# Kernel optimization log

Hardware: AMD Instinct MI355X
Metric: run time of the kernel (lower is better)

Reference implementation:

```python
import jax, jax.numpy as jnp
import numpy as np

# levels for the auction iterations: j = 7..-1 gives level = -4^j, j = -2 gives level = 0
_LEVEL_JS = list(range(7, -3, -1))


def approx_match(xyz1, xyz2):
    # xyz1: [B,N,3], xyz2: [B,M,3] -> soft match matrix [B,N,M]
    B, N, _ = xyz1.shape
    M = xyz2.shape[1]
    multiL = 1.0 if N >= M else float(M // N)
    multiR = float(N // M) if N >= M else 1.0
    # pairwise squared distances [B,N,M]
    d2 = jnp.sum((xyz1[:, :, None, :] - xyz2[:, None, :, :]) ** 2, axis=-1)
    levels = jnp.array([0.0 if j == -2 else -(4.0 ** j) for j in _LEVEL_JS],
                       dtype=xyz1.dtype)

    def step(carry, level):
        match, remainL, remainR = carry
        w = jnp.exp(level * d2) * remainR[:, None, :]                      # [B,N,M]
        # row-normalize to each left point's remaining mass
        w = w * (remainL / (jnp.sum(w, axis=2) + 1e-9))[:, :, None]
        # clip columns to right points' remaining capacity
        ss = jnp.sum(w, axis=1) + 1e-9                                     # [B,M]
        w = w * jnp.minimum(remainR / ss, 1.0)[:, None, :]
        match = match + w
        remainL = jnp.maximum(remainL - jnp.sum(w, axis=2), 0.0)
        remainR = jnp.maximum(remainR - jnp.sum(w, axis=1), 0.0)
        return (match, remainL, remainR), None

    init = (jnp.zeros_like(d2),
            jnp.full((B, N), multiL, dtype=d2.dtype),
            jnp.full((B, M), multiR, dtype=d2.dtype))
    (match, _, _), _ = jax.lax.scan(step, init, levels)
    return match


def match_cost(xyz1, xyz2, match):
    # cost[b] = sum_{k,l} match[b,k,l] * ||xyz1[b,k] - xyz2[b,l]||
    d = jnp.sqrt(jnp.sum((xyz1[:, :, None, :] - xyz2[:, None, :, :]) ** 2, axis=-1))
    return jnp.sum(match * d, axis=(1, 2))


def setup_inputs() -> dict:
    key = jax.random.key(0)
    k1, k2 = jax.random.split(key)
    B, N, M = 8, 2048, 2048
    input1 = jax.random.normal(k1, (B, N, 3), dtype=jnp.float32)
    input2 = jax.random.normal(k2, (B, M, 3), dtype=jnp.float32)
    return {"input1": input1, "input2": input2}


def reference(input1, input2):
    match = approx_match(input1, input2)
    return match_cost(input1, input2, match)
```

## Files before the change

kernel.cpp:

```cpp
#include <hip/hip_runtime.h>
#include <hip/hip_fp16.h>


#define BATCH 8
#define NPTS 2048
#define MPTS 2048
#define BLOCK 1024
#define ROWS 64
#define BLOCKS_PER_BATCH 32
#define NSUB 8
#define SUBTGT (BLOCKS_PER_BATCH / NSUB)
#define NSYNC 21
#define PAD 16
#define SROW 17
#define LOG2E 1.44269504088896340736f

__device__ __forceinline__ float fast_exp2(float x) {
  return __builtin_amdgcn_exp2f(x);
}
__device__ __forceinline__ float fast_sqrt(float a) {
  return __builtin_amdgcn_sqrtf(a);
}
__device__ __forceinline__ float packh2(float c, float r) {
  __half2 h = __halves2half2(__float2half_rn(c), __float2half_rn(r));
  return __builtin_bit_cast(float, h);
}

__device__ __forceinline__ float cohLoad(const float* p) {
  return __hip_atomic_load((float*)p, __ATOMIC_RELAXED,
                           __HIP_MEMORY_SCOPE_AGENT);
}
__device__ __forceinline__ void cohStore(float* p, float v) {
  __hip_atomic_store(p, v, __ATOMIC_RELAXED, __HIP_MEMORY_SCOPE_AGENT);
}
__device__ __forceinline__ float4 cohLoad4(const float4* p) {
  const float* f = (const float*)p;
  return make_float4(cohLoad(f), cohLoad(f + 1), cohLoad(f + 2),
                     cohLoad(f + 3));
}

__device__ __forceinline__ void lds_barrier() {
  asm volatile("s_waitcnt lgkmcnt(0)" ::: "memory");
  __builtin_amdgcn_s_barrier();
  __builtin_amdgcn_sched_barrier(0);
}

__device__ __forceinline__ void batch_barrier(unsigned* base, int bid) {
  __syncthreads();
  if (threadIdx.x == 0) {
    __hip_atomic_fetch_add(base + (bid & (NSUB - 1)) * PAD, 1u,
                           __ATOMIC_RELAXED, __HIP_MEMORY_SCOPE_AGENT);
  }
  if (threadIdx.x < NSUB) {
    int guard = 0;
    while (__hip_atomic_load(base + threadIdx.x * PAD, __ATOMIC_RELAXED,
                             __HIP_MEMORY_SCOPE_AGENT) < (unsigned)SUBTGT) {
      __builtin_amdgcn_s_sleep(2);
      if (++guard > (1 << 22)) break;
    }
  }
  asm volatile("" ::: "memory");
  __syncthreads();
}

__device__ __forceinline__ void load8(const float4* q, int r0,
                                      float* x, float* y, float* z) {
  int b4 = (r0 >> 2) * 3;
  float4 q0 = q[b4], q1 = q[b4 + 1], q2 = q[b4 + 2];
  float4 q3 = q[b4 + 3], q4 = q[b4 + 4], q5 = q[b4 + 5];
  x[0] = q0.x; y[0] = q0.y; z[0] = q0.z;
  x[1] = q0.w; y[1] = q1.x; z[1] = q1.y;
  x[2] = q1.z; y[2] = q1.w; z[2] = q2.x;
  x[3] = q2.y; y[3] = q2.z; z[3] = q2.w;
  x[4] = q3.x; y[4] = q3.y; z[4] = q3.z;
  x[5] = q3.w; y[5] = q4.x; z[5] = q4.y;
  x[6] = q4.z; y[6] = q4.w; z[6] = q5.x;
  x[7] = q5.y; y[7] = q5.z; z[7] = q5.w;
}

__device__ __forceinline__ void sweep2T_fuse(
    float nc, int tid, int t0, const float4* q1, const float* rsG,
    float* wpB, const float4* sP, float4* sStage, float* sRR) {
  const int m_idx = tid >> 4, c = tid & 15;
  const float4 pm = sP[t0 + m_idx];
  const float4* rsg4 = (const float4*)rsG;
  const int rowb = c * SROW;
  const int tl = tid & 255;
  const int qtr = tid >> 8;
  const bool isXyz = tl < 192;
  const int t = tl - 192;
  const int wIdx = qtr * (16 * SROW) +
                   (isXyz ? ((tl / 12) * SROW + (tl % 12))
                          : ((t >> 2) * SROW + 12 + (t & 3)));
  float4 v = isXyz ? q1[qtr * 192 + tl] : cohLoad4(rsg4 + qtr * 64 + t);
  float part = 0.f;
  for (int r = 0; r < 2; ++r) {
    lds_barrier();
    sStage[wIdx] = v;
    if (r < 1) {
      int ch = 4 + qtr;
      v = isXyz ? q1[ch * 192 + tl] : cohLoad4(rsg4 + ch * 64 + t);
    }
    lds_barrier();
#pragma unroll
    for (int h = 0; h < 4; ++h) {
      const float4* sB = sStage + h * (16 * SROW);
#pragma unroll
      for (int k = 0; k < 4; ++k) {
        float4 a  = sB[rowb + 3 * k];
        float4 bb = sB[rowb + 3 * k + 1];
        float4 cc = sB[rowb + 3 * k + 2];
        float4 r4 = sB[rowb + 12 + k];
        float px[4] = {a.x, a.w, bb.z, cc.y};
        float py[4] = {a.y, bb.x, bb.w, cc.z};
        float pz[4] = {a.z, bb.y, cc.x, cc.w};
        float rr[4] = {r4.x, r4.y, r4.z, r4.w};
#pragma unroll
        for (int j = 0; j < 4; ++j) {
          float dx = px[j] - pm.x, dy = py[j] - pm.y, dz = pz[j] - pm.z;
          float d2 = __builtin_fmaf(dx, dx, __builtin_fmaf(dy, dy, dz * dz));
          part = __builtin_fmaf(fast_exp2(nc * d2), rr[j], part);
        }
      }
    }
  }
  part += __shfl_xor(part, 1, 64);
  part += __shfl_xor(part, 2, 64);
  part += __shfl_xor(part, 4, 64);
  part += __shfl_xor(part, 8, 64);
  if (c == 0) {
    float t1v = part;
    float rr = sRR[m_idx];
    float colsum = rr * t1v;
    float cs = fminf(rr / (colsum + 1e-9f), 1.0f);
    float ccv = rr * cs;
    float rn = fmaxf(rr - colsum * cs, 0.f);
    cohStore(wpB + t0 + m_idx, packh2(ccv, rn));
    sRR[m_idx] = rn;
  }
}

__global__ __launch_bounds__(BLOCK, 4) void emd_fused_kernel(
    const float* __restrict__ xyz1, const float* __restrict__ xyz2,
    float* __restrict__ out, float* __restrict__ rowscaleG,
    float* __restrict__ wPack, float* __restrict__ R9acc,
    float* __restrict__ t9, float* __restrict__ outAcc,
    unsigned* __restrict__ ctr) {
  __shared__ float4 sP[MPTS];
  __shared__ float4 sStage[4 * 16 * SROW];
  __shared__ float sRedS[ROWS * 4];
  __shared__ float sRedC[ROWS * 4];
  __shared__ float sRedR[ROWS * 4];
  __shared__ float sCost[ROWS];
  __shared__ float sRowScale[ROWS];
  __shared__ float sRemainL[ROWS];
  __shared__ float sRR[ROWS];

  const int tid = threadIdx.x;
  const int bid = blockIdx.x;
  const int b = bid >> 5;
  const int t0 = (bid & 31) * ROWS;
  const bool desig = (bid & 31) == 0;
  const int wave = tid >> 6, lane = tid & 63;
  const int mq = wave & 3;
  const int rh = wave >> 2;
  const size_t bM = (size_t)b * MPTS;
  float costAcc = 0.f;

  float* rsG = rowscaleG + (size_t)b * NPTS;
  float* wpB = wPack + bM;
  const float4* q1 = (const float4*)(xyz1 + (size_t)b * NPTS * 3);
  const float4* q2 = (const float4*)(xyz2 + bM * 3);
#define CTRB(s) (ctr + (size_t)(((s) * BATCH + b) * NSUB) * PAD)

  if (tid < MPTS / 4) {
    int g = tid;
    float4 a = q2[3 * g], bb = q2[3 * g + 1], c = q2[3 * g + 2];
    sP[4 * g + 0] = make_float4(a.x, a.y, a.z, 0.f);
    sP[4 * g + 1] = make_float4(a.w, bb.x, bb.y, 0.f);
    sP[4 * g + 2] = make_float4(bb.z, bb.w, c.x, 0.f);
    sP[4 * g + 3] = make_float4(c.y, c.z, c.w, 0.f);
  }
  if (tid < ROWS) sRR[tid] = 1.0f;
  if (desig && tid == 0) {
    cohStore(R9acc + b * PAD, 0.f);
    cohStore(t9 + b * PAD, 0.f);
    cohStore(outAcc + b * PAD, 0.f);
  }
  __syncthreads();

  const float nc0 = -16384.0f * LOG2E;
  {
    const int ph = lane >> 1, rg = lane & 1;
    float x1a[8], y1a[8], z1a[8], acc[8];
    load8(q1, t0 + rh * 16 + rg * 8, x1a, y1a, z1a);
#pragma unroll
    for (int j = 0; j < 8; ++j) acc[j] = 0.f;
    const int mb = mq * 512 + ph;
#pragma unroll 2
    for (int it = 0; it < 16; ++it) {
      float4 v = sP[mb + it * 32];
#pragma unroll
      for (int j = 0; j < 8; ++j) {
        float dx = x1a[j] - v.x, dy = y1a[j] - v.y, dz = z1a[j] - v.z;
        float d2 = __builtin_fmaf(dx, dx, __builtin_fmaf(dy, dy, dz * dz));
        acc[j] += fast_exp2(nc0 * d2);
      }
    }
#pragma unroll
    for (int j = 0; j < 8; ++j) {
      acc[j] += __shfl_xor(acc[j], 2, 64);
      acc[j] += __shfl_xor(acc[j], 4, 64);
      acc[j] += __shfl_xor(acc[j], 8, 64);
      acc[j] += __shfl_xor(acc[j], 16, 64);
      acc[j] += __shfl_xor(acc[j], 32, 64);
    }
    if (lane < 2) {
#pragma unroll
      for (int j = 0; j < 8; ++j)
        sRedS[(rh * 16 + rg * 8 + j) * 4 + mq] = acc[j];
    }
    __syncthreads();
    if (tid < ROWS) {
      float s = sRedS[tid * 4] + sRedS[tid * 4 + 1] + sRedS[tid * 4 + 2] +
                sRedS[tid * 4 + 3];
      float rs = 1.0f / (s + 1e-9f);
      sRowScale[tid] = rs;
      cohStore(rsG + t0 + tid, rs);
    }
  }
  batch_barrier(CTRB(0), bid);
  sweep2T_fuse(nc0, tid, t0, q1, rsG, wpB, sP, sStage, sRR);
  batch_barrier(CTRB(1), bid);

  float x1[4], y1[4], z1[4];
  {
    int b4 = ((t0 + rh * 16 + (lane & 3) * 4) >> 2) * 3;
    float4 a = q1[b4], bb = q1[b4 + 1], c = q1[b4 + 2];
    x1[0] = a.x;  y1[0] = a.y;  z1[0] = a.z;
    x1[1] = a.w;  y1[1] = bb.x; z1[1] = bb.y;
    x1[2] = bb.z; y1[2] = bb.w; z1[2] = c.x;
    x1[3] = c.y;  y1[3] = c.z;  z1[3] = c.w;
  }
  const int phc = lane >> 2, rgc = lane & 3;
  const int mbc = mq * 512 + phc;

  float nc2 = -4096.0f * LOG2E;
  for (int l = 0; l < 9; ++l) {
    const bool LAST = (l == 8);
#pragma unroll
    for (int k = 0; k < 2; ++k) {
      int m = tid + k * 1024;
      sP[m].w = cohLoad(wpB + m);
    }
    __syncthreads();
    float accS[4] = {0.f, 0.f, 0.f, 0.f};
    float accC[4] = {0.f, 0.f, 0.f, 0.f};
    float accR[4] = {0.f, 0.f, 0.f, 0.f};
#pragma unroll 4
    for (int it = 0; it < 32; ++it) {
      float4 v = sP[mbc + it * 16];
      __half2 h = __builtin_bit_cast(__half2, v.w);
      float cc = __low2float(h);
      float rr = __high2float(h);
#pragma unroll
      for (int j = 0; j < 4; ++j) {
        float dx = x1[j] - v.x, dy = y1[j] - v.y, dz = z1[j] - v.z;
        float d2 = __builtin_fmaf(dx, dx, __builtin_fmaf(dy, dy, dz * dz));
        float sq = fast_sqrt(d2);
        float e2 = fast_exp2(nc2 * d2);
        float e2s = e2 * e2;
        float e1 = e2s * e2s;
        float t = e1 * cc;
        accS[j] += t;
        accC[j] = __builtin_fmaf(t, sq, accC[j]);
        accR[j] = __builtin_fmaf(e2, rr, accR[j]);
      }
    }
#pragma unroll
    for (int j = 0; j < 4; ++j) {
      accS[j] += __shfl_xor(accS[j], 4, 64);
      accS[j] += __shfl_xor(accS[j], 8, 64);
      accS[j] += __shfl_xor(accS[j], 16, 64);
      accS[j] += __shfl_xor(accS[j], 32, 64);
      accC[j] += __shfl_xor(accC[j], 4, 64);
      accC[j] += __shfl_xor(accC[j], 8, 64);
      accC[j] += __shfl_xor(accC[j], 16, 64);
      accC[j] += __shfl_xor(accC[j], 32, 64);
      accR[j] += __shfl_xor(accR[j], 4, 64);
      accR[j] += __shfl_xor(accR[j], 8, 64);
      accR[j] += __shfl_xor(accR[j], 16, 64);
      accR[j] += __shfl_xor(accR[j], 32, 64);
    }
    if (lane < 4) {
#pragma unroll
      for (int j = 0; j < 4; ++j) {
        int row = rh * 16 + rgc * 4 + j;
        sRedS[row * 4 + mq] = accS[j];
        sRedC[row * 4 + mq] = accC[j];
        sRedR[row * 4 + mq] = accR[j];
      }
    }
    __syncthreads();
    if (tid < ROWS) {
      float S2 = sRedS[tid * 4] + sRedS[tid * 4 + 1] + sRedS[tid * 4 + 2] +
                 sRedS[tid * 4 + 3];
      float C = sRedC[tid * 4] + sRedC[tid * 4 + 1] + sRedC[tid * 4 + 2] +
                sRedC[tid * 4 + 3];
      float R = sRedR[tid * 4] + sRedR[tid * 4 + 1] + sRedR[tid * 4 + 2] +
                sRedR[tid * 4 + 3];
      if (LAST) R = cohLoad(R9acc + b * PAD);
      float rs = sRowScale[tid];
      float rl = (l == 0) ? 1.0f : sRemainL[tid];
      float rlN = fmaxf(rl - rs * S2, 0.f);
      sRemainL[tid] = rlN;
      float rsN = rlN / (R + 1e-9f);
      sRowScale[tid] = rsN;
      if (!LAST) cohStore(rsG + t0 + tid, rsN);
      sCost[tid] = rs * C;
    }
    __syncthreads();
    if (tid == 0) {
      float t = 0.f;
#pragma unroll
      for (int i = 0; i < ROWS; ++i) t += sCost[i];
      costAcc += t;
      if (LAST) {
        float r = 0.f;
#pragma unroll
        for (int i = 0; i < ROWS; ++i) r += sRowScale[i];
        atomicAdd(t9 + b * PAD, r);
      }
    }
    if (!LAST) {
      batch_barrier(CTRB(2 + 2 * l), bid);
      sweep2T_fuse(nc2, tid, t0, q1, rsG, wpB, sP, sStage, sRR);
      if (l == 7) {
        __syncthreads();
        if (tid == 0) {
          float r9 = 0.f;
#pragma unroll
          for (int i = 0; i < ROWS; ++i) r9 += sRR[i];
          atomicAdd(R9acc + b * PAD, r9);
        }
      }
      batch_barrier(CTRB(3 + 2 * l), bid);
      nc2 *= 0.25f;
    }
  }
  batch_barrier(CTRB(18), bid);

  if (tid < ROWS) {
    float rr = sRR[tid];
    float t1s = cohLoad(t9 + b * PAD);
    float w = rr * fminf(rr / (__builtin_fmaf(rr, t1s, 1e-9f)), 1.0f);
    cohStore(wpB + t0 + tid, w);
  }
  batch_barrier(CTRB(19), bid);

  {
#pragma unroll
    for (int k = 0; k < 2; ++k) {
      int m = tid + k * 1024;
      sP[m].w = cohLoad(wpB + m);
    }
    __syncthreads();
    const int ph = lane >> 1, rg = lane & 1;
    float x1a[8], y1a[8], z1a[8], acc[8];
    load8(q1, t0 + rh * 16 + rg * 8, x1a, y1a, z1a);
#pragma unroll
    for (int j = 0; j < 8; ++j) acc[j] = 0.f;
    const int mb = mq * 512 + ph;
#pragma unroll 2
    for (int it = 0; it < 16; ++it) {
      float4 v = sP[mb + it * 32];
#pragma unroll
      for (int j = 0; j < 8; ++j) {
        float dx = x1a[j] - v.x, dy = y1a[j] - v.y, dz = z1a[j] - v.z;
        float d2 = __builtin_fmaf(dx, dx, __builtin_fmaf(dy, dy, dz * dz));
        acc[j] = __builtin_fmaf(fast_sqrt(d2), v.w, acc[j]);
      }
    }
#pragma unroll
    for (int j = 0; j < 8; ++j) {
      acc[j] += __shfl_xor(acc[j], 2, 64);
      acc[j] += __shfl_xor(acc[j], 4, 64);
      acc[j] += __shfl_xor(acc[j], 8, 64);
      acc[j] += __shfl_xor(acc[j], 16, 64);
      acc[j] += __shfl_xor(acc[j], 32, 64);
    }
    if (lane < 2) {
#pragma unroll
      for (int j = 0; j < 8; ++j)
        sRedS[(rh * 16 + rg * 8 + j) * 4 + mq] = acc[j];
    }
    __syncthreads();
    if (tid < ROWS) {
      float C = sRedS[tid * 4] + sRedS[tid * 4 + 1] + sRedS[tid * 4 + 2] +
                sRedS[tid * 4 + 3];
      sCost[tid] = sRowScale[tid] * C;
    }
    __syncthreads();
    if (tid == 0) {
      float t = 0.f;
#pragma unroll
      for (int i = 0; i < ROWS; ++i) t += sCost[i];
      costAcc += t;
      atomicAdd(outAcc + b * PAD, costAcc);
    }
  }
  batch_barrier(CTRB(20), bid);
  if (desig && tid == 0) out[b] = cohLoad(outAcc + b * PAD);
#undef CTRB
}

extern "C" void kernel_launch(void* const* d_in, const int* in_sizes, int n_in,
                              void* d_out, int out_size, void* d_ws, size_t ws_size,
                              hipStream_t stream) {
  const float* xyz1 = (const float*)d_in[0];
  const float* xyz2 = (const float*)d_in[1];
  float* out = (float*)d_out;
  float* ws = (float*)d_ws;

  const int BM = BATCH * MPTS;
  float* rowscaleG = ws;
  float* wPack     = ws + BM;
  float* R9acc     = ws + 2 * BM;
  float* t9        = ws + 2 * BM + BATCH * PAD;
  float* outAcc    = ws + 2 * BM + 2 * BATCH * PAD;
  unsigned* ctr    = (unsigned*)(ws + 2 * BM + 3 * BATCH * PAD);

  hipMemsetAsync(ctr, 0, (size_t)NSYNC * BATCH * NSUB * PAD * sizeof(unsigned),
                 stream);

  void* args[] = {(void*)&xyz1, (void*)&xyz2, (void*)&out, (void*)&rowscaleG,
                  (void*)&wPack, (void*)&R9acc, (void*)&t9, (void*)&outAcc,
                  (void*)&ctr};
  hipLaunchKernel((const void*)emd_fused_kernel,
                  dim3(BATCH * (NPTS / ROWS)), dim3(BLOCK), args, 0, stream);
}
```

Before: 312.5 us.

## Sort points by x in-kernel and skip tiles whose exp underflows

Each block bitonic-sorts both point clouds by x coordinate in LDS and stages the sorted points. It then computes per-tile x bounds for the left and right points. In the dense passes and in the column sweep, whole tiles are skipped when the minimum x-gap makes the exponent fall below -130, where the fp32 exp2 contribution is effectively zero. This targets the large share of wasted exp work at the sharp early levels. The cost is an in-kernel sort on every block, branch divergence, and a larger 64 KB dynamic LDS allocation that may lower occupancy.

```diff
diff --git a/kernel.cpp b/kernel.cpp
--- a/kernel.cpp
+++ b/kernel.cpp
@@ -12,7 +12,7 @@
 #define SUBTGT (BLOCKS_PER_BATCH / NSUB)
 #define NSYNC 21
 #define PAD 16
-#define SROW 17
+#define SKIP_THR (-130.0f)
 #define LOG2E 1.44269504088896340736f
 
 __device__ __forceinline__ float fast_exp2(float x) {
@@ -32,17 +32,6 @@
 }
 __device__ __forceinline__ void cohStore(float* p, float v) {
   __hip_atomic_store(p, v, __ATOMIC_RELAXED, __HIP_MEMORY_SCOPE_AGENT);
-}
-__device__ __forceinline__ float4 cohLoad4(const float4* p) {
-  const float* f = (const float*)p;
-  return make_float4(cohLoad(f), cohLoad(f + 1), cohLoad(f + 2),
-                     cohLoad(f + 3));
-}
-
-__device__ __forceinline__ void lds_barrier() {
-  asm volatile("s_waitcnt lgkmcnt(0)" ::: "memory");
-  __builtin_amdgcn_s_barrier();
-  __builtin_amdgcn_sched_barrier(0);
 }
 
 __device__ __forceinline__ void batch_barrier(unsigned* base, int bid) {
@@ -63,65 +52,45 @@
   __syncthreads();
 }
 
-__device__ __forceinline__ void load8(const float4* q, int r0,
-                                      float* x, float* y, float* z) {
-  int b4 = (r0 >> 2) * 3;
-  float4 q0 = q[b4], q1 = q[b4 + 1], q2 = q[b4 + 2];
-  float4 q3 = q[b4 + 3], q4 = q[b4 + 4], q5 = q[b4 + 5];
-  x[0] = q0.x; y[0] = q0.y; z[0] = q0.z;
-  x[1] = q0.w; y[1] = q1.x; z[1] = q1.y;
-  x[2] = q1.z; y[2] = q1.w; z[2] = q2.x;
-  x[3] = q2.y; y[3] = q2.z; z[3] = q2.w;
-  x[4] = q3.x; y[4] = q3.y; z[4] = q3.z;
-  x[5] = q3.w; y[5] = q4.x; z[5] = q4.y;
-  x[6] = q4.z; y[6] = q4.w; z[6] = q5.x;
-  x[7] = q5.y; y[7] = q5.z; z[7] = q5.w;
+__device__ __forceinline__ void wave_interval(float& lo, float& hi) {
+#pragma unroll
+  for (int s = 1; s < 64; s <<= 1) {
+    lo = fminf(lo, __shfl_xor(lo, s, 64));
+    hi = fmaxf(hi, __shfl_xor(hi, s, 64));
+  }
+}
+
+__device__ __forceinline__ void load8L(const float4* sA, int r0,
+                                       float* x, float* y, float* z) {
+#pragma unroll
+  for (int j = 0; j < 8; ++j) {
+    float4 v = sA[r0 + j];
+    x[j] = v.x; y[j] = v.y; z[j] = v.z;
+  }
 }
 
 __device__ __forceinline__ void sweep2T_fuse(
-    float nc, int tid, int t0, const float4* q1, const float* rsG,
-    float* wpB, const float4* sP, float4* sStage, float* sRR) {
+    float nc, int tid, int t0, const float* rsG, float* wpB,
+    float4* sA, const float4* sP, const float2* sTileN, float* sRR) {
+  sA[tid].w = cohLoad(rsG + tid);
+  sA[tid + 1024].w = cohLoad(rsG + tid + 1024);
+  __syncthreads();
   const int m_idx = tid >> 4, c = tid & 15;
   const float4 pm = sP[t0 + m_idx];
-  const float4* rsg4 = (const float4*)rsG;
-  const int rowb = c * SROW;
-  const int tl = tid & 255;
-  const int qtr = tid >> 8;
-  const bool isXyz = tl < 192;
-  const int t = tl - 192;
-  const int wIdx = qtr * (16 * SROW) +
-                   (isXyz ? ((tl / 12) * SROW + (tl % 12))
-                          : ((t >> 2) * SROW + 12 + (t & 3)));
-  float4 v = isXyz ? q1[qtr * 192 + tl] : cohLoad4(rsg4 + qtr * 64 + t);
+  float mlo = pm.x, mhi = pm.x;
+  wave_interval(mlo, mhi);
   float part = 0.f;
-  for (int r = 0; r < 2; ++r) {
-    lds_barrier();
-    sStage[wIdx] = v;
-    if (r < 1) {
-      int ch = 4 + qtr;
-      v = isXyz ? q1[ch * 192 + tl] : cohLoad4(rsg4 + ch * 64 + t);
-    }
-    lds_barrier();
-#pragma unroll
-    for (int h = 0; h < 4; ++h) {
-      const float4* sB = sStage + h * (16 * SROW);
-#pragma unroll
-      for (int k = 0; k < 4; ++k) {
-        float4 a  = sB[rowb + 3 * k];
-        float4 bb = sB[rowb + 3 * k + 1];
-        float4 cc = sB[rowb + 3 * k + 2];
-        float4 r4 = sB[rowb + 12 + k];
-        float px[4] = {a.x, a.w, bb.z, cc.y};
-        float py[4] = {a.y, bb.x, bb.w, cc.z};
-        float pz[4] = {a.z, bb.y, cc.x, cc.w};
-        float rr[4] = {r4.x, r4.y, r4.z, r4.w};
-#pragma unroll
-        for (int j = 0; j < 4; ++j) {
-          float dx = px[j] - pm.x, dy = py[j] - pm.y, dz = pz[j] - pm.z;
-          float d2 = __builtin_fmaf(dx, dx, __builtin_fmaf(dy, dy, dz * dz));
-          part = __builtin_fmaf(fast_exp2(nc * d2), rr[j], part);
-        }
-      }
+  for (int ch = 0; ch < 32; ++ch) {
+    float2 tn = sTileN[ch];
+    float gap = fmaxf(0.f, fmaxf(tn.x - mhi, mlo - tn.y));
+    if (nc * gap * gap < SKIP_THR) continue;
+    int nb = ch * 64 + c;
+#pragma unroll
+    for (int j = 0; j < 4; ++j) {
+      float4 v = sA[nb + 16 * j];
+      float dx = v.x - pm.x, dy = v.y - pm.y, dz = v.z - pm.z;
+      float d2 = __builtin_fmaf(dx, dx, __builtin_fmaf(dy, dy, dz * dz));
+      part = __builtin_fmaf(fast_exp2(nc * d2), v.w, part);
     }
   }
   part += __shfl_xor(part, 1, 64);
@@ -140,14 +109,18 @@
   }
 }
 
-__global__ __launch_bounds__(BLOCK, 4) void emd_fused_kernel(
+__global__ __launch_bounds__(BLOCK) void emd_fused_kernel(
     const float* __restrict__ xyz1, const float* __restrict__ xyz2,
     float* __restrict__ out, float* __restrict__ rowscaleG,
     float* __restrict__ wPack, float* __restrict__ R9acc,
     float* __restrict__ t9, float* __restrict__ outAcc,
     unsigned* __restrict__ ctr) {
-  __shared__ float4 sP[MPTS];
-  __shared__ float4 sStage[4 * 16 * SROW];
+  extern __shared__ __align__(16) float4 sDyn[];
+  float4* sA = sDyn;
+  float4* sP = sDyn + 2048;
+  unsigned* sKeyA = (unsigned*)(sDyn + 2048);
+  unsigned* sKeyB = ((unsigned*)(sDyn + 2048)) + 2048;
+
   __shared__ float sRedS[ROWS * 4];
   __shared__ float sRedC[ROWS * 4];
   __shared__ float sRedR[ROWS * 4];
@@ -155,6 +128,8 @@
   __shared__ float sRowScale[ROWS];
   __shared__ float sRemainL[ROWS];
   __shared__ float sRR[ROWS];
+  __shared__ float2 sTileM[128];
+  __shared__ float2 sTileN[32];
 
   const int tid = threadIdx.x;
   const int bid = blockIdx.x;
@@ -169,17 +144,42 @@
 
   float* rsG = rowscaleG + (size_t)b * NPTS;
   float* wpB = wPack + bM;
-  const float4* q1 = (const float4*)(xyz1 + (size_t)b * NPTS * 3);
-  const float4* q2 = (const float4*)(xyz2 + bM * 3);
+  const float* p1 = xyz1 + (size_t)b * NPTS * 3;
+  const float* p2 = xyz2 + bM * 3;
 #define CTRB(s) (ctr + (size_t)(((s) * BATCH + b) * NSUB) * PAD)
 
-  if (tid < MPTS / 4) {
-    int g = tid;
-    float4 a = q2[3 * g], bb = q2[3 * g + 1], c = q2[3 * g + 2];
-    sP[4 * g + 0] = make_float4(a.x, a.y, a.z, 0.f);
-    sP[4 * g + 1] = make_float4(a.w, bb.x, bb.y, 0.f);
-    sP[4 * g + 2] = make_float4(bb.z, bb.w, c.x, 0.f);
-    sP[4 * g + 3] = make_float4(c.y, c.z, c.w, 0.f);
+  for (int e = tid; e < 2048; e += 1024) {
+    unsigned u1 = __builtin_bit_cast(unsigned, p1[e * 3]);
+    u1 = (u1 & 0x80000000u) ? ~u1 : (u1 | 0x80000000u);
+    sKeyA[e] = (u1 & 0xFFFFF800u) | (unsigned)e;
+    unsigned u2 = __builtin_bit_cast(unsigned, p2[e * 3]);
+    u2 = (u2 & 0x80000000u) ? ~u2 : (u2 | 0x80000000u);
+    sKeyB[e] = (u2 & 0xFFFFF800u) | (unsigned)e;
+  }
+  for (unsigned k = 2; k <= 2048; k <<= 1) {
+    for (unsigned j = k >> 1; j > 0; j >>= 1) {
+      __syncthreads();
+      for (int e = tid; e < 2048; e += 1024) {
+        int l = e ^ (int)j;
+        if (l > e) {
+          bool up = ((e & (int)k) == 0);
+          unsigned a = sKeyA[e], bv = sKeyA[l];
+          if ((a > bv) == up) { sKeyA[e] = bv; sKeyA[l] = a; }
+          unsigned a2 = sKeyB[e], b2 = sKeyB[l];
+          if ((a2 > b2) == up) { sKeyB[e] = b2; sKeyB[l] = a2; }
+        }
+      }
+    }
+  }
+  __syncthreads();
+  {
+    int iA0 = sKeyA[tid] & 2047, iA1 = sKeyA[tid + 1024] & 2047;
+    int iB0 = sKeyB[tid] & 2047, iB1 = sKeyB[tid + 1024] & 2047;
+    __syncthreads();
+    sA[tid]        = make_float4(p1[iA0*3], p1[iA0*3+1], p1[iA0*3+2], 0.f);
+    sA[tid + 1024] = make_float4(p1[iA1*3], p1[iA1*3+1], p1[iA1*3+2], 0.f);
+    sP[tid]        = make_float4(p2[iB0*3], p2[iB0*3+1], p2[iB0*3+2], 0.f);
+    sP[tid + 1024] = make_float4(p2[iB1*3], p2[iB1*3+1], p2[iB1*3+2], 0.f);
   }
   if (tid < ROWS) sRR[tid] = 1.0f;
   if (desig && tid == 0) {
@@ -188,17 +188,43 @@
     cohStore(outAcc + b * PAD, 0.f);
   }
   __syncthreads();
+  if (tid < 128) {
+    float lo = sP[tid * 16].x, hi = lo;
+    for (int i = 1; i < 16; ++i) {
+      float x = sP[tid * 16 + i].x;
+      lo = fminf(lo, x); hi = fmaxf(hi, x);
+    }
+    sTileM[tid] = make_float2(lo, hi);
+  } else if (tid < 160) {
+    int t = tid - 128;
+    float lo = sA[t * 64].x, hi = lo;
+    for (int i = 1; i < 64; ++i) {
+      float x = sA[t * 64 + i].x;
+      lo = fminf(lo, x); hi = fmaxf(hi, x);
+    }
+    sTileN[t] = make_float2(lo, hi);
+  }
+  __syncthreads();
 
   const float nc0 = -16384.0f * LOG2E;
   {
     const int ph = lane >> 1, rg = lane & 1;
     float x1a[8], y1a[8], z1a[8], acc[8];
-    load8(q1, t0 + rh * 16 + rg * 8, x1a, y1a, z1a);
+    load8L(sA, t0 + rh * 16 + rg * 8, x1a, y1a, z1a);
 #pragma unroll
     for (int j = 0; j < 8; ++j) acc[j] = 0.f;
+    float rlo = x1a[0], rhi = x1a[0];
+#pragma unroll
+    for (int j = 1; j < 8; ++j) {
+      rlo = fminf(rlo, x1a[j]); rhi = fmaxf(rhi, x1a[j]);
+    }
+    wave_interval(rlo, rhi);
     const int mb = mq * 512 + ph;
-#pragma unroll 2
     for (int it = 0; it < 16; ++it) {
+      int tb = mq * 32 + it * 2;
+      float lo = sTileM[tb].x, hi = sTileM[tb + 1].y;
+      float gap = fmaxf(0.f, fmaxf(lo - rhi, rlo - hi));
+      if (nc0 * gap * gap < SKIP_THR) continue;
       float4 v = sP[mb + it * 32];
 #pragma unroll
       for (int j = 0; j < 8; ++j) {
@@ -230,18 +256,21 @@
     }
   }
   batch_barrier(CTRB(0), bid);
-  sweep2T_fuse(nc0, tid, t0, q1, rsG, wpB, sP, sStage, sRR);
+  sweep2T_fuse(nc0, tid, t0, rsG, wpB, sA, sP, sTileN, sRR);
   batch_barrier(CTRB(1), bid);
 
   float x1[4], y1[4], z1[4];
   {
-    int b4 = ((t0 + rh * 16 + (lane & 3) * 4) >> 2) * 3;
-    float4 a = q1[b4], bb = q1[b4 + 1], c = q1[b4 + 2];
-    x1[0] = a.x;  y1[0] = a.y;  z1[0] = a.z;
-    x1[1] = a.w;  y1[1] = bb.x; z1[1] = bb.y;
-    x1[2] = bb.z; y1[2] = bb.w; z1[2] = c.x;
-    x1[3] = c.y;  y1[3] = c.z;  z1[3] = c.w;
-  }
+    int r0 = t0 + rh * 16 + (lane & 3) * 4;
+#pragma unroll
+    for (int j = 0; j < 4; ++j) {
+      float4 v = sA[r0 + j];
+      x1[j] = v.x; y1[j] = v.y; z1[j] = v.z;
+    }
+  }
+  float rlo = fminf(fminf(x1[0], x1[1]), fminf(x1[2], x1[3]));
+  float rhi = fmaxf(fmaxf(x1[0], x1[1]), fmaxf(x1[2], x1[3]));
+  wave_interval(rlo, rhi);
   const int phc = lane >> 2, rgc = lane & 3;
   const int mbc = mq * 512 + phc;
 
@@ -257,8 +286,10 @@
     float accS[4] = {0.f, 0.f, 0.f, 0.f};
     float accC[4] = {0.f, 0.f, 0.f, 0.f};
     float accR[4] = {0.f, 0.f, 0.f, 0.f};
-#pragma unroll 4
     for (int it = 0; it < 32; ++it) {
+      float2 tm = sTileM[mq * 32 + it];
+      float gap = fmaxf(0.f, fmaxf(tm.x - rhi, rlo - tm.y));
+      if (nc2 * gap * gap < SKIP_THR) continue;
       float4 v = sP[mbc + it * 16];
       __half2 h = __builtin_bit_cast(__half2, v.w);
       float cc = __low2float(h);
@@ -334,7 +365,7 @@
     }
     if (!LAST) {
       batch_barrier(CTRB(2 + 2 * l), bid);
-      sweep2T_fuse(nc2, tid, t0, q1, rsG, wpB, sP, sStage, sRR);
+      sweep2T_fuse(nc2, tid, t0, rsG, wpB, sA, sP, sTileN, sRR);
       if (l == 7) {
         __syncthreads();
         if (tid == 0) {
@@ -367,7 +398,7 @@
     __syncthreads();
     const int ph = lane >> 1, rg = lane & 1;
     float x1a[8], y1a[8], z1a[8], acc[8];
-    load8(q1, t0 + rh * 16 + rg * 8, x1a, y1a, z1a);
+    load8L(sA, t0 + rh * 16 + rg * 8, x1a, y1a, z1a);
 #pragma unroll
     for (int j = 0; j < 8; ++j) acc[j] = 0.f;
     const int mb = mq * 512 + ph;
@@ -430,6 +461,13 @@
   float* outAcc    = ws + 2 * BM + 2 * BATCH * PAD;
   unsigned* ctr    = (unsigned*)(ws + 2 * BM + 3 * BATCH * PAD);
 
+  static bool attrSet = false;
+  if (!attrSet) {
+    hipFuncSetAttribute((const void*)emd_fused_kernel,
+                        hipFuncAttributeMaxDynamicSharedMemorySize, 65536);
+    attrSet = true;
+  }
+
   hipMemsetAsync(ctr, 0, (size_t)NSYNC * BATCH * NSUB * PAD * sizeof(unsigned),
                  stream);
 
@@ -437,5 +475,6 @@
                   (void*)&wPack, (void*)&R9acc, (void*)&t9, (void*)&outAcc,
                   (void*)&ctr};
   hipLaunchKernel((const void*)emd_fused_kernel,
-                  dim3(BATCH * (NPTS / ROWS)), dim3(BLOCK), args, 0, stream);
-}
+                  dim3(BATCH * (NPTS / ROWS)), dim3(BLOCK), args,
+                  65536, stream);
+}
```

Result: slower. 353.2 us (+13.0%).
